# Kernel tuning notes

Measured on AMD Instinct MI355X. Metric: run time of the kernel, lower is better.

The kernel has to match this reference:

```python
import jax, jax.numpy as jnp
import numpy as np

VOCAB = 100000
EMB = 256
HID = 512
HDIR = HID // 2
T = 10            # tagset size
START = 8
STOP = 9
S = 4096          # sequence length
NEG = -10000.0


def setup_inputs() -> dict:
    key = jax.random.key(0)
    ks = jax.random.split(key, 16)
    sentence = jax.random.randint(ks[0], (S,), 0, VOCAB)
    emb = jax.random.normal(ks[1], (VOCAB, EMB), dtype=jnp.float32) * 0.02
    s = 1.0 / np.sqrt(HDIR).astype(np.float32)

    def lstm_weights(k):
        k1, k2, k3, k4 = jax.random.split(k, 4)
        return (
            jax.random.uniform(k1, (4 * HDIR, EMB), jnp.float32, -s, s),
            jax.random.uniform(k2, (4 * HDIR, HDIR), jnp.float32, -s, s),
            jax.random.uniform(k3, (4 * HDIR,), jnp.float32, -s, s),
            jax.random.uniform(k4, (4 * HDIR,), jnp.float32, -s, s),
        )

    Wih_f, Whh_f, bih_f, bhh_f = lstm_weights(ks[2])
    Wih_b, Whh_b, bih_b, bhh_b = lstm_weights(ks[3])
    so = 1.0 / np.sqrt(HID).astype(np.float32)
    W_out = jax.random.uniform(ks[4], (T, HID), jnp.float32, -so, so)
    b_out = jax.random.uniform(ks[5], (T,), jnp.float32, -so, so)
    transitions = jax.random.normal(ks[6], (T, T), dtype=jnp.float32)
    transitions = transitions.at[START, :].set(NEG).at[:, STOP].set(NEG)
    return {
        "sentence": sentence, "emb": emb,
        "Wih_f": Wih_f, "Whh_f": Whh_f, "bih_f": bih_f, "bhh_f": bhh_f,
        "Wih_b": Wih_b, "Whh_b": Whh_b, "bih_b": bih_b, "bhh_b": bhh_b,
        "W_out": W_out, "b_out": b_out, "transitions": transitions,
    }


def _lstm_dir(x, Wih, Whh, bih, bhh):
    # x: [S, EMB] -> hidden states [S, HDIR]; PyTorch gate order i,f,g,o
    b = bih + bhh
    xW = x @ Wih.T + b  # precompute input contribution: [S, 4*HDIR]

    def step(carry, xw_t):
        h, c = carry
        z = xw_t + Whh @ h
        i, f, g, o = jnp.split(z, 4)
        i = jax.nn.sigmoid(i); f = jax.nn.sigmoid(f)
        g = jnp.tanh(g); o = jax.nn.sigmoid(o)
        c = f * c + i * g
        h = o * jnp.tanh(c)
        return (h, c), h

    h0 = jnp.zeros((HDIR,), x.dtype)
    _, hs = jax.lax.scan(step, (h0, h0), xW)
    return hs


def _viterbi(feats, transitions):
    # feats: [S, T]
    def vstep(fv, feat):
        ntv = fv[None, :] + transitions        # [T(next), T(prev)]
        bp = jnp.argmax(ntv, axis=1)           # [T]
        fv_new = jnp.max(ntv, axis=1) + feat   # [T]
        return fv_new, bp

    init = jnp.full((T,), NEG, feats.dtype).at[START].set(0.0)
    fv, bps = jax.lax.scan(vstep, init, feats)
    terminal = fv + transitions[STOP]
    best = jnp.argmax(terminal)
    score = terminal[best]

    def back(tag, bp):
        return bp[tag], tag

    _, path_rev = jax.lax.scan(back, best, bps[::-1])
    return score, path_rev[::-1]


def reference(sentence, emb, Wih_f, Whh_f, bih_f, bhh_f,
              Wih_b, Whh_b, bih_b, bhh_b, W_out, b_out, transitions):
    x = emb[sentence]                                   # [S, EMB]
    h_f = _lstm_dir(x, Wih_f, Whh_f, bih_f, bhh_f)      # [S, HDIR]
    h_b = _lstm_dir(x[::-1], Wih_b, Whh_b, bih_b, bhh_b)[::-1]
    lstm_out = jnp.concatenate([h_f, h_b], axis=-1)     # [S, HID]
    feats = lstm_out @ W_out.T + b_out                  # [S, T]
    score, path = _viterbi(feats, transitions)
    return score, path
```

## Files before the change

kernel.cpp:

```cpp
#include <hip/hip_runtime.h>
#include <math.h>

#define S_LEN 4096
#define HDIRC 256
#define NTAG 10
#define START_TAG 8
#define STOP_TAG 9
#define NEGV -10000.0f

#define XW_OFF 0UL
#define XW_SZ  (2UL * S_LEN * 1024)
#define HS_OFF (XW_OFF + XW_SZ)
#define HS_SZ  (2UL * S_LEN * 256)
#define WT_OFF (HS_OFF + HS_SZ)
#define WT_SZ  (2UL * 256 * 1024)
#define FE_OFF (WT_OFF + WT_SZ)
#define FE_SZ  ((size_t)S_LEN * NTAG)
#define RING_OFF (FE_OFF + FE_SZ)
#define RING_SZ (2UL * 2 * 256 * 2)

__global__ void transpose_wih(const float* __restrict__ wf,
                              const float* __restrict__ wb,
                              float* __restrict__ wT) {
    __shared__ float tile[32][33];
    const float* src = blockIdx.z ? wb : wf;
    float* dst = wT + (size_t)blockIdx.z * 256 * 1024;
    int x = blockIdx.x * 32 + threadIdx.x;
    int y = blockIdx.y * 32 + threadIdx.y;
    tile[threadIdx.y][threadIdx.x] = src[y * 256 + x];
    __syncthreads();
    int ko = blockIdx.x * 32 + threadIdx.y;
    int ro = blockIdx.y * 32 + threadIdx.x;
    dst[(size_t)ko * 1024 + ro] = tile[threadIdx.x][threadIdx.y];
}

__global__ __launch_bounds__(256) void xw_gemm(
    const int* __restrict__ sent, const float* __restrict__ emb,
    const float* __restrict__ wT,
    const float* __restrict__ bih_f, const float* __restrict__ bhh_f,
    const float* __restrict__ bih_b, const float* __restrict__ bhh_b,
    float* __restrict__ xw) {
    int dir = blockIdx.y;
    int t0 = blockIdx.x * 16;
    int tid = threadIdx.x;
    __shared__ __align__(16) float xs[16][256];
    for (int i = 0; i < 16; ++i) {
        int t = t0 + i;
        int pos = dir ? (S_LEN - 1 - t) : t;
        int idx = sent[pos];
        xs[i][tid] = emb[(size_t)idx * 256 + tid];
    }
    __syncthreads();
    const float* w = wT + (size_t)dir * 256 * 1024;
    const float* bi = dir ? bih_b : bih_f;
    const float* bh = dir ? bhh_b : bhh_f;
    float4 bv;
    bv.x = bi[4 * tid + 0] + bh[4 * tid + 0];
    bv.y = bi[4 * tid + 1] + bh[4 * tid + 1];
    bv.z = bi[4 * tid + 2] + bh[4 * tid + 2];
    bv.w = bi[4 * tid + 3] + bh[4 * tid + 3];
    float4 acc[16];
#pragma unroll
    for (int i = 0; i < 16; ++i) acc[i] = bv;
    for (int k4 = 0; k4 < 64; ++k4) {
        float4 w0 = ((const float4*)(w + (size_t)(4 * k4 + 0) * 1024))[tid];
        float4 w1 = ((const float4*)(w + (size_t)(4 * k4 + 1) * 1024))[tid];
        float4 w2 = ((const float4*)(w + (size_t)(4 * k4 + 2) * 1024))[tid];
        float4 w3 = ((const float4*)(w + (size_t)(4 * k4 + 3) * 1024))[tid];
#pragma unroll
        for (int i = 0; i < 16; ++i) {
            float4 xv = *(const float4*)&xs[i][4 * k4];
            acc[i].x = fmaf(w0.x, xv.x, acc[i].x);
            acc[i].y = fmaf(w0.y, xv.x, acc[i].y);
            acc[i].z = fmaf(w0.z, xv.x, acc[i].z);
            acc[i].w = fmaf(w0.w, xv.x, acc[i].w);
            acc[i].x = fmaf(w1.x, xv.y, acc[i].x);
            acc[i].y = fmaf(w1.y, xv.y, acc[i].y);
            acc[i].z = fmaf(w1.z, xv.y, acc[i].z);
            acc[i].w = fmaf(w1.w, xv.y, acc[i].w);
            acc[i].x = fmaf(w2.x, xv.z, acc[i].x);
            acc[i].y = fmaf(w2.y, xv.z, acc[i].y);
            acc[i].z = fmaf(w2.z, xv.z, acc[i].z);
            acc[i].w = fmaf(w2.w, xv.z, acc[i].w);
            acc[i].x = fmaf(w3.x, xv.w, acc[i].x);
            acc[i].y = fmaf(w3.y, xv.w, acc[i].y);
            acc[i].z = fmaf(w3.z, xv.w, acc[i].z);
            acc[i].w = fmaf(w3.w, xv.w, acc[i].w);
        }
    }
#pragma unroll
    for (int i = 0; i < 16; ++i)
        ((float4*)(xw + ((size_t)dir * S_LEN + t0 + i) * 1024))[tid] = acc[i];
}

__global__ __launch_bounds__(256, 1) void lstm_rec(
    const float* __restrict__ whh_f, const float* __restrict__ whh_b,
    const float* __restrict__ xw, float* __restrict__ hs,
    unsigned long long* __restrict__ ring) {
    int blk = blockIdx.x;
    int dir = blk >> 4;
    int b = blk & 15;
    int tid = threadIdx.x;
    int g = tid >> 6;
    int lane = tid & 63;
    int v = lane >> 2;
    int u = lane & 3;

    const float* whh = dir ? whh_b : whh_f;
    float4 w[4][4];
#pragma unroll
    for (int j = 0; j < 4; ++j)
#pragma unroll
        for (int i = 0; i < 4; ++i)
            w[j][i] = *(const float4*)(whh +
                (size_t)(g * 256 + b * 16 + 4 * u + j) * 256 + 16 * v + 4 * i);
#pragma unroll
    for (int j = 0; j < 4; ++j)
#pragma unroll
        for (int i = 0; i < 4; ++i)
            asm volatile("" : "+v"(w[j][i].x), "+v"(w[j][i].y),
                              "+v"(w[j][i].z), "+v"(w[j][i].w));

    const float* xwd = xw + (size_t)dir * S_LEN * 1024;
    float* hsd = hs + (size_t)dir * S_LEN * 256;
    unsigned long long* ringd = ring + dir * 512;

    __shared__ __align__(16) float hbf[320];
    __shared__ __align__(16) float zpart[1056];
    for (int i = tid; i < 320; i += 256) hbf[i] = 0.f;
    float c = 0.f;
    int crow = (lane >> 4) * 256 + b * 16 + (lane & 15);
    float xw_cur = (g == 0) ? xwd[crow] : 0.f;
    __syncthreads();

    for (int t = 0; t < S_LEN; ++t) {
        const float4* hb4 = (const float4*)hbf + v * 5;
        float4 h0 = hb4[0], h1 = hb4[1], h2 = hb4[2], h3 = hb4[3];
        float s0, s1, s2, s3;
        {
            float4 a0, a1, a2, a3;
            a0.x = w[0][0].x * h0.x; a0.y = w[0][0].y * h0.y;
            a0.z = w[0][0].z * h0.z; a0.w = w[0][0].w * h0.w;
            a1.x = w[1][0].x * h0.x; a1.y = w[1][0].y * h0.y;
            a1.z = w[1][0].z * h0.z; a1.w = w[1][0].w * h0.w;
            a2.x = w[2][0].x * h0.x; a2.y = w[2][0].y * h0.y;
            a2.z = w[2][0].z * h0.z; a2.w = w[2][0].w * h0.w;
            a3.x = w[3][0].x * h0.x; a3.y = w[3][0].y * h0.y;
            a3.z = w[3][0].z * h0.z; a3.w = w[3][0].w * h0.w;

            a0.x = fmaf(w[0][1].x, h1.x, a0.x); a0.y = fmaf(w[0][1].y, h1.y, a0.y);
            a0.z = fmaf(w[0][1].z, h1.z, a0.z); a0.w = fmaf(w[0][1].w, h1.w, a0.w);
            a1.x = fmaf(w[1][1].x, h1.x, a1.x); a1.y = fmaf(w[1][1].y, h1.y, a1.y);
            a1.z = fmaf(w[1][1].z, h1.z, a1.z); a1.w = fmaf(w[1][1].w, h1.w, a1.w);
            a2.x = fmaf(w[2][1].x, h1.x, a2.x); a2.y = fmaf(w[2][1].y, h1.y, a2.y);
            a2.z = fmaf(w[2][1].z, h1.z, a2.z); a2.w = fmaf(w[2][1].w, h1.w, a2.w);
            a3.x = fmaf(w[3][1].x, h1.x, a3.x); a3.y = fmaf(w[3][1].y, h1.y, a3.y);
            a3.z = fmaf(w[3][1].z, h1.z, a3.z); a3.w = fmaf(w[3][1].w, h1.w, a3.w);

            a0.x = fmaf(w[0][2].x, h2.x, a0.x); a0.y = fmaf(w[0][2].y, h2.y, a0.y);
            a0.z = fmaf(w[0][2].z, h2.z, a0.z); a0.w = fmaf(w[0][2].w, h2.w, a0.w);
            a1.x = fmaf(w[1][2].x, h2.x, a1.x); a1.y = fmaf(w[1][2].y, h2.y, a1.y);
            a1.z = fmaf(w[1][2].z, h2.z, a1.z); a1.w = fmaf(w[1][2].w, h2.w, a1.w);
            a2.x = fmaf(w[2][2].x, h2.x, a2.x); a2.y = fmaf(w[2][2].y, h2.y, a2.y);
            a2.z = fmaf(w[2][2].z, h2.z, a2.z); a2.w = fmaf(w[2][2].w, h2.w, a2.w);
            a3.x = fmaf(w[3][2].x, h2.x, a3.x); a3.y = fmaf(w[3][2].y, h2.y, a3.y);
            a3.z = fmaf(w[3][2].z, h2.z, a3.z); a3.w = fmaf(w[3][2].w, h2.w, a3.w);

            a0.x = fmaf(w[0][3].x, h3.x, a0.x); a0.y = fmaf(w[0][3].y, h3.y, a0.y);
            a0.z = fmaf(w[0][3].z, h3.z, a0.z); a0.w = fmaf(w[0][3].w, h3.w, a0.w);
            a1.x = fmaf(w[1][3].x, h3.x, a1.x); a1.y = fmaf(w[1][3].y, h3.y, a1.y);
            a1.z = fmaf(w[1][3].z, h3.z, a1.z); a1.w = fmaf(w[1][3].w, h3.w, a1.w);
            a2.x = fmaf(w[2][3].x, h3.x, a2.x); a2.y = fmaf(w[2][3].y, h3.y, a2.y);
            a2.z = fmaf(w[2][3].z, h3.z, a2.z); a2.w = fmaf(w[2][3].w, h3.w, a2.w);
            a3.x = fmaf(w[3][3].x, h3.x, a3.x); a3.y = fmaf(w[3][3].y, h3.y, a3.y);
            a3.z = fmaf(w[3][3].z, h3.z, a3.z); a3.w = fmaf(w[3][3].w, h3.w, a3.w);

            s0 = (a0.x + a0.y) + (a0.z + a0.w);
            s1 = (a1.x + a1.y) + (a1.z + a1.w);
            s2 = (a2.x + a2.y) + (a2.z + a2.w);
            s3 = (a3.x + a3.y) + (a3.z + a3.w);
        }
        *(float4*)&zpart[g * 264 + v * 16 + u * 4] = make_float4(s0, s1, s2, s3);
        __syncthreads();

        if (g == 0) {
            int g2 = lane >> 4, s = lane & 15;
            const float* zp = &zpart[g2 * 264 + s];
            float z = xw_cur;
#pragma unroll
            for (int vv = 0; vv < 16; ++vv) z += zp[vv * 16];
            int tn = (t + 1 < S_LEN) ? t + 1 : t;
            float xw_next = xwd[(size_t)tn * 1024 + crow];
            float act = (g2 == 2) ? tanhf(z) : 1.f / (1.f + expf(-z));
            float fg = __shfl(act, (lane & 15) + 16, 64);
            float gg = __shfl(act, (lane & 15) + 32, 64);
            float og = __shfl(act, (lane & 15) + 48, 64);
            unsigned long long* slot = ringd + (size_t)(t & 1) * 256;
            unsigned int want = (unsigned int)(t + 1);
            if (lane < 16) {
                c = fmaf(fg, c, act * gg);
                float h = og * tanhf(c);
                hsd[(size_t)t * 256 + b * 16 + lane] = h;
                unsigned long long pk = ((unsigned long long)want << 32) |
                                        (unsigned long long)__float_as_uint(h);
                __hip_atomic_store(&slot[b * 16 + lane], pk,
                                   __ATOMIC_RELAXED, __HIP_MEMORY_SCOPE_AGENT);
            }
            unsigned long long v0, v1, v2, v3;
            for (;;) {
                v0 = __hip_atomic_load(&slot[lane], __ATOMIC_RELAXED, __HIP_MEMORY_SCOPE_AGENT);
                v1 = __hip_atomic_load(&slot[lane + 64], __ATOMIC_RELAXED, __HIP_MEMORY_SCOPE_AGENT);
                v2 = __hip_atomic_load(&slot[lane + 128], __ATOMIC_RELAXED, __HIP_MEMORY_SCOPE_AGENT);
                v3 = __hip_atomic_load(&slot[lane + 192], __ATOMIC_RELAXED, __HIP_MEMORY_SCOPE_AGENT);
                bool ok = ((unsigned int)(v0 >> 32) == want) &
                          ((unsigned int)(v1 >> 32) == want) &
                          ((unsigned int)(v2 >> 32) == want) &
                          ((unsigned int)(v3 >> 32) == want);
                if (__all(ok)) break;
            }
            int sl = lane & 15, ch = lane >> 4;
            hbf[(ch + 0) * 20 + sl]  = __uint_as_float((unsigned int)v0);
            hbf[(ch + 4) * 20 + sl]  = __uint_as_float((unsigned int)v1);
            hbf[(ch + 8) * 20 + sl]  = __uint_as_float((unsigned int)v2);
            hbf[(ch + 12) * 20 + sl] = __uint_as_float((unsigned int)v3);
            xw_cur = xw_next;
        }
        __syncthreads();
    }
}

__global__ __launch_bounds__(64) void feats_k(const float* __restrict__ hs,
                                              const float* __restrict__ wout,
                                              const float* __restrict__ bout,
                                              float* __restrict__ feats) {
    int t = blockIdx.x, tau = blockIdx.y, lane = threadIdx.x;
    const float* hf = hs + (size_t)t * 256;
    const float* hbk = hs + (size_t)S_LEN * 256 + (size_t)(S_LEN - 1 - t) * 256;
    const float* w = wout + (size_t)tau * 512;
    float s = 0.f;
#pragma unroll
    for (int m = 0; m < 4; ++m) s = fmaf(w[lane + 64 * m], hf[lane + 64 * m], s);
#pragma unroll
    for (int m = 0; m < 4; ++m) s = fmaf(w[256 + lane + 64 * m], hbk[lane + 64 * m], s);
#pragma unroll
    for (int off = 32; off > 0; off >>= 1) s += __shfl_down(s, off, 64);
    if (lane == 0) feats[(size_t)t * NTAG + tau] = s + bout[tau];
}

__global__ __launch_bounds__(64) void viterbi_k(const float* __restrict__ feats,
                                                const float* __restrict__ trans,
                                                float* __restrict__ out) {
    __shared__ float fstage[128 * NTAG];
    __shared__ unsigned char bp[S_LEN * NTAG];
    __shared__ float path[S_LEN];
    __shared__ float fvbuf[NTAG];
    __shared__ float term[NTAG];
    int tid = threadIdx.x;
    float tr[NTAG];
    float trstop = 0.f;
    if (tid < NTAG) {
#pragma unroll
        for (int j = 0; j < NTAG; ++j) tr[j] = trans[tid * NTAG + j];
        trstop = trans[STOP_TAG * NTAG + tid];
    }
    float fv = (tid == START_TAG) ? 0.f : NEGV;
    for (int t0 = 0; t0 < S_LEN; t0 += 128) {
        __syncthreads();
        for (int i = tid; i < 128 * NTAG; i += 64) fstage[i] = feats[(size_t)t0 * NTAG + i];
        __syncthreads();
        for (int tt = 0; tt < 128; ++tt) {
            int t = t0 + tt;
            if (tid < NTAG) fvbuf[tid] = fv;
            __syncthreads();
            if (tid < NTAG) {
                float best = -3.4e38f; int bj = 0;
#pragma unroll
                for (int j = 0; j < NTAG; ++j) {
                    float v = fvbuf[j] + tr[j];
                    if (v > best) { best = v; bj = j; }
                }
                bp[t * NTAG + tid] = (unsigned char)bj;
                fv = best + fstage[tt * NTAG + tid];
            }
            __syncthreads();
        }
    }
    if (tid < NTAG) term[tid] = fv + trstop;
    __syncthreads();
    if (tid == 0) {
        float best = -3.4e38f; int bi = 0;
#pragma unroll
        for (int i = 0; i < NTAG; ++i) {
            float v = term[i];
            if (v > best) { best = v; bi = i; }
        }
        out[0] = best;
        int tag = bi;
        for (int t = S_LEN - 1; t >= 0; --t) {
            path[t] = (float)tag;
            tag = bp[t * NTAG + tag];
        }
    }
    __syncthreads();
    for (int i = tid; i < S_LEN; i += 64) out[1 + i] = path[i];
}

extern "C" void kernel_launch(void* const* d_in, const int* in_sizes, int n_in,
                              void* d_out, int out_size, void* d_ws, size_t ws_size,
                              hipStream_t stream) {
    const int* sent = (const int*)d_in[0];
    const float* emb = (const float*)d_in[1];
    const float* wih_f = (const float*)d_in[2];
    const float* whh_f = (const float*)d_in[3];
    const float* bih_f = (const float*)d_in[4];
    const float* bhh_f = (const float*)d_in[5];
    const float* wih_b = (const float*)d_in[6];
    const float* whh_b = (const float*)d_in[7];
    const float* bih_b = (const float*)d_in[8];
    const float* bhh_b = (const float*)d_in[9];
    const float* wout = (const float*)d_in[10];
    const float* bout = (const float*)d_in[11];
    const float* trans = (const float*)d_in[12];

    float* ws = (float*)d_ws;
    float* xw = ws + XW_OFF;
    float* hs = ws + HS_OFF;
    float* wT = ws + WT_OFF;
    float* fe = ws + FE_OFF;
    unsigned long long* ring = (unsigned long long*)(ws + RING_OFF);

    hipLaunchKernelGGL(transpose_wih, dim3(8, 32, 2), dim3(32, 32), 0, stream,
                       wih_f, wih_b, wT);
    hipLaunchKernelGGL(xw_gemm, dim3(S_LEN / 16, 2), dim3(256), 0, stream,
                       sent, emb, wT, bih_f, bhh_f, bih_b, bhh_b, xw);
    hipLaunchKernelGGL(lstm_rec, dim3(32), dim3(256), 0, stream,
                       whh_f, whh_b, xw, hs, ring);
    hipLaunchKernelGGL(feats_k, dim3(S_LEN, NTAG), dim3(64), 0, stream,
                       hs, wout, bout, fe);
    hipLaunchKernelGGL(viterbi_k, dim3(1), dim3(64), 0, stream,
                       fe, trans, (float*)d_out);
}
```

Baseline: 7.548 ms.

## Make each wavefront self-sufficient in LSTM recurrence, removing block barriers

Each wavefront now owns complete gate rows for 4 hidden units. It reduces the 256-wide dot product with cross-lane shuffles instead of a shared-memory partial-sum buffer. Every wavefront computes its own cell update, publishes h to the global ring and polls the ring into a private shared-memory copy of h. This removes both per-step __syncthreads and the serial gate-reduction phase on a single wave. In exchange there are 4x more pollers on the ring and every wave reloads the full h vector.

```diff
diff --git a/kernel.cpp b/kernel.cpp
--- a/kernel.cpp
+++ b/kernel.cpp
@@ -101,131 +101,87 @@
     int dir = blk >> 4;
     int b = blk & 15;
     int tid = threadIdx.x;
-    int g = tid >> 6;
-    int lane = tid & 63;
-    int v = lane >> 2;
-    int u = lane & 3;
+    int wv = tid >> 6;
+    int l = tid & 63;
+    int q = l >> 4;
+    int r = l & 15;
+    int g = r >> 2;
+    int dl = r & 3;
 
     const float* whh = dir ? whh_b : whh_f;
-    float4 w[4][4];
-#pragma unroll
-    for (int j = 0; j < 4; ++j)
-#pragma unroll
-        for (int i = 0; i < 4; ++i)
-            w[j][i] = *(const float4*)(whh +
-                (size_t)(g * 256 + b * 16 + 4 * u + j) * 256 + 16 * v + 4 * i);
-#pragma unroll
-    for (int j = 0; j < 4; ++j)
-#pragma unroll
-        for (int i = 0; i < 4; ++i)
-            asm volatile("" : "+v"(w[j][i].x), "+v"(w[j][i].y),
-                              "+v"(w[j][i].z), "+v"(w[j][i].w));
+    int row = g * 256 + b * 16 + 4 * wv + dl;
+    float4 w[16];
+#pragma unroll
+    for (int i = 0; i < 16; ++i)
+        w[i] = *(const float4*)(whh + (size_t)row * 256 + 64 * q + 4 * i);
+#pragma unroll
+    for (int i = 0; i < 16; ++i)
+        asm volatile("" : "+v"(w[i].x), "+v"(w[i].y), "+v"(w[i].z), "+v"(w[i].w));
 
     const float* xwd = xw + (size_t)dir * S_LEN * 1024;
     float* hsd = hs + (size_t)dir * S_LEN * 256;
     unsigned long long* ringd = ring + dir * 512;
 
-    __shared__ __align__(16) float hbf[320];
-    __shared__ __align__(16) float zpart[1056];
-    for (int i = tid; i < 320; i += 256) hbf[i] = 0.f;
+    __shared__ __align__(16) float hb[4][272];
+    float* hbw = hb[wv];
+    hbw[l] = 0.f; hbw[68 + l] = 0.f; hbw[136 + l] = 0.f; hbw[204 + l] = 0.f;
+    const float4* hq = (const float4*)(hbw + 68 * q);
+
     float c = 0.f;
-    int crow = (lane >> 4) * 256 + b * 16 + (lane & 15);
-    float xw_cur = (g == 0) ? xwd[crow] : 0.f;
-    __syncthreads();
+    int hdim = b * 16 + 4 * wv + dl;
+    float xw_cur = xwd[row];
 
     for (int t = 0; t < S_LEN; ++t) {
-        const float4* hb4 = (const float4*)hbf + v * 5;
-        float4 h0 = hb4[0], h1 = hb4[1], h2 = hb4[2], h3 = hb4[3];
-        float s0, s1, s2, s3;
-        {
-            float4 a0, a1, a2, a3;
-            a0.x = w[0][0].x * h0.x; a0.y = w[0][0].y * h0.y;
-            a0.z = w[0][0].z * h0.z; a0.w = w[0][0].w * h0.w;
-            a1.x = w[1][0].x * h0.x; a1.y = w[1][0].y * h0.y;
-            a1.z = w[1][0].z * h0.z; a1.w = w[1][0].w * h0.w;
-            a2.x = w[2][0].x * h0.x; a2.y = w[2][0].y * h0.y;
-            a2.z = w[2][0].z * h0.z; a2.w = w[2][0].w * h0.w;
-            a3.x = w[3][0].x * h0.x; a3.y = w[3][0].y * h0.y;
-            a3.z = w[3][0].z * h0.z; a3.w = w[3][0].w * h0.w;
-
-            a0.x = fmaf(w[0][1].x, h1.x, a0.x); a0.y = fmaf(w[0][1].y, h1.y, a0.y);
-            a0.z = fmaf(w[0][1].z, h1.z, a0.z); a0.w = fmaf(w[0][1].w, h1.w, a0.w);
-            a1.x = fmaf(w[1][1].x, h1.x, a1.x); a1.y = fmaf(w[1][1].y, h1.y, a1.y);
-            a1.z = fmaf(w[1][1].z, h1.z, a1.z); a1.w = fmaf(w[1][1].w, h1.w, a1.w);
-            a2.x = fmaf(w[2][1].x, h1.x, a2.x); a2.y = fmaf(w[2][1].y, h1.y, a2.y);
-            a2.z = fmaf(w[2][1].z, h1.z, a2.z); a2.w = fmaf(w[2][1].w, h1.w, a2.w);
-            a3.x = fmaf(w[3][1].x, h1.x, a3.x); a3.y = fmaf(w[3][1].y, h1.y, a3.y);
-            a3.z = fmaf(w[3][1].z, h1.z, a3.z); a3.w = fmaf(w[3][1].w, h1.w, a3.w);
-
-            a0.x = fmaf(w[0][2].x, h2.x, a0.x); a0.y = fmaf(w[0][2].y, h2.y, a0.y);
-            a0.z = fmaf(w[0][2].z, h2.z, a0.z); a0.w = fmaf(w[0][2].w, h2.w, a0.w);
-            a1.x = fmaf(w[1][2].x, h2.x, a1.x); a1.y = fmaf(w[1][2].y, h2.y, a1.y);
-            a1.z = fmaf(w[1][2].z, h2.z, a1.z); a1.w = fmaf(w[1][2].w, h2.w, a1.w);
-            a2.x = fmaf(w[2][2].x, h2.x, a2.x); a2.y = fmaf(w[2][2].y, h2.y, a2.y);
-            a2.z = fmaf(w[2][2].z, h2.z, a2.z); a2.w = fmaf(w[2][2].w, h2.w, a2.w);
-            a3.x = fmaf(w[3][2].x, h2.x, a3.x); a3.y = fmaf(w[3][2].y, h2.y, a3.y);
-            a3.z = fmaf(w[3][2].z, h2.z, a3.z); a3.w = fmaf(w[3][2].w, h2.w, a3.w);
-
-            a0.x = fmaf(w[0][3].x, h3.x, a0.x); a0.y = fmaf(w[0][3].y, h3.y, a0.y);
-            a0.z = fmaf(w[0][3].z, h3.z, a0.z); a0.w = fmaf(w[0][3].w, h3.w, a0.w);
-            a1.x = fmaf(w[1][3].x, h3.x, a1.x); a1.y = fmaf(w[1][3].y, h3.y, a1.y);
-            a1.z = fmaf(w[1][3].z, h3.z, a1.z); a1.w = fmaf(w[1][3].w, h3.w, a1.w);
-            a2.x = fmaf(w[2][3].x, h3.x, a2.x); a2.y = fmaf(w[2][3].y, h3.y, a2.y);
-            a2.z = fmaf(w[2][3].z, h3.z, a2.z); a2.w = fmaf(w[2][3].w, h3.w, a2.w);
-            a3.x = fmaf(w[3][3].x, h3.x, a3.x); a3.y = fmaf(w[3][3].y, h3.y, a3.y);
-            a3.z = fmaf(w[3][3].z, h3.z, a3.z); a3.w = fmaf(w[3][3].w, h3.w, a3.w);
-
-            s0 = (a0.x + a0.y) + (a0.z + a0.w);
-            s1 = (a1.x + a1.y) + (a1.z + a1.w);
-            s2 = (a2.x + a2.y) + (a2.z + a2.w);
-            s3 = (a3.x + a3.y) + (a3.z + a3.w);
-        }
-        *(float4*)&zpart[g * 264 + v * 16 + u * 4] = make_float4(s0, s1, s2, s3);
-        __syncthreads();
-
-        if (g == 0) {
-            int g2 = lane >> 4, s = lane & 15;
-            const float* zp = &zpart[g2 * 264 + s];
-            float z = xw_cur;
-#pragma unroll
-            for (int vv = 0; vv < 16; ++vv) z += zp[vv * 16];
-            int tn = (t + 1 < S_LEN) ? t + 1 : t;
-            float xw_next = xwd[(size_t)tn * 1024 + crow];
-            float act = (g2 == 2) ? tanhf(z) : 1.f / (1.f + expf(-z));
-            float fg = __shfl(act, (lane & 15) + 16, 64);
-            float gg = __shfl(act, (lane & 15) + 32, 64);
-            float og = __shfl(act, (lane & 15) + 48, 64);
-            unsigned long long* slot = ringd + (size_t)(t & 1) * 256;
-            unsigned int want = (unsigned int)(t + 1);
-            if (lane < 16) {
-                c = fmaf(fg, c, act * gg);
-                float h = og * tanhf(c);
-                hsd[(size_t)t * 256 + b * 16 + lane] = h;
-                unsigned long long pk = ((unsigned long long)want << 32) |
-                                        (unsigned long long)__float_as_uint(h);
-                __hip_atomic_store(&slot[b * 16 + lane], pk,
-                                   __ATOMIC_RELAXED, __HIP_MEMORY_SCOPE_AGENT);
-            }
-            unsigned long long v0, v1, v2, v3;
-            for (;;) {
-                v0 = __hip_atomic_load(&slot[lane], __ATOMIC_RELAXED, __HIP_MEMORY_SCOPE_AGENT);
-                v1 = __hip_atomic_load(&slot[lane + 64], __ATOMIC_RELAXED, __HIP_MEMORY_SCOPE_AGENT);
-                v2 = __hip_atomic_load(&slot[lane + 128], __ATOMIC_RELAXED, __HIP_MEMORY_SCOPE_AGENT);
-                v3 = __hip_atomic_load(&slot[lane + 192], __ATOMIC_RELAXED, __HIP_MEMORY_SCOPE_AGENT);
-                bool ok = ((unsigned int)(v0 >> 32) == want) &
-                          ((unsigned int)(v1 >> 32) == want) &
-                          ((unsigned int)(v2 >> 32) == want) &
-                          ((unsigned int)(v3 >> 32) == want);
-                if (__all(ok)) break;
-            }
-            int sl = lane & 15, ch = lane >> 4;
-            hbf[(ch + 0) * 20 + sl]  = __uint_as_float((unsigned int)v0);
-            hbf[(ch + 4) * 20 + sl]  = __uint_as_float((unsigned int)v1);
-            hbf[(ch + 8) * 20 + sl]  = __uint_as_float((unsigned int)v2);
-            hbf[(ch + 12) * 20 + sl] = __uint_as_float((unsigned int)v3);
-            xw_cur = xw_next;
-        }
-        __syncthreads();
+        float4 acc = make_float4(0.f, 0.f, 0.f, 0.f);
+#pragma unroll
+        for (int i = 0; i < 16; ++i) {
+            float4 h4 = hq[i];
+            acc.x = fmaf(w[i].x, h4.x, acc.x);
+            acc.y = fmaf(w[i].y, h4.y, acc.y);
+            acc.z = fmaf(w[i].z, h4.z, acc.z);
+            acc.w = fmaf(w[i].w, h4.w, acc.w);
+        }
+        float z = (acc.x + acc.y) + (acc.z + acc.w);
+        z += __shfl_xor(z, 16, 64);
+        z += __shfl_xor(z, 32, 64);
+        z += xw_cur;
+        float act = (g == 2) ? tanhf(z) : 1.f / (1.f + expf(-z));
+        int base = l & 48;
+        float ig = __shfl(act, base + dl, 64);
+        float fg = __shfl(act, base + 4 + dl, 64);
+        float gg = __shfl(act, base + 8 + dl, 64);
+        float og = __shfl(act, base + 12 + dl, 64);
+        c = fmaf(fg, c, ig * gg);
+        float h = og * tanhf(c);
+
+        unsigned long long* slot = ringd + (size_t)(t & 1) * 256;
+        unsigned int want = (unsigned int)(t + 1);
+        if (l < 4) {
+            unsigned long long pk = ((unsigned long long)want << 32) |
+                                    (unsigned long long)__float_as_uint(h);
+            __hip_atomic_store(&slot[hdim], pk,
+                               __ATOMIC_RELAXED, __HIP_MEMORY_SCOPE_AGENT);
+        }
+        int tn = (t + 1 < S_LEN) ? t + 1 : t;
+        float xw_next = xwd[(size_t)tn * 1024 + row];
+        if (l < 4) hsd[(size_t)t * 256 + hdim] = h;
+        unsigned long long v0, v1, v2, v3;
+        for (;;) {
+            v0 = __hip_atomic_load(&slot[l], __ATOMIC_RELAXED, __HIP_MEMORY_SCOPE_AGENT);
+            v1 = __hip_atomic_load(&slot[l + 64], __ATOMIC_RELAXED, __HIP_MEMORY_SCOPE_AGENT);
+            v2 = __hip_atomic_load(&slot[l + 128], __ATOMIC_RELAXED, __HIP_MEMORY_SCOPE_AGENT);
+            v3 = __hip_atomic_load(&slot[l + 192], __ATOMIC_RELAXED, __HIP_MEMORY_SCOPE_AGENT);
+            bool ok = ((unsigned int)(v0 >> 32) == want) &
+                      ((unsigned int)(v1 >> 32) == want) &
+                      ((unsigned int)(v2 >> 32) == want) &
+                      ((unsigned int)(v3 >> 32) == want);
+            if (__all(ok)) break;
+        }
+        hbw[l] = __uint_as_float((unsigned int)v0);
+        hbw[68 + l] = __uint_as_float((unsigned int)v1);
+        hbw[136 + l] = __uint_as_float((unsigned int)v2);
+        hbw[204 + l] = __uint_as_float((unsigned int)v3);
+        xw_cur = xw_next;
     }
 }
 
```

After: 12.47 ms. 65.2% more time.
